# Kernel optimization log

Measured on AMD Instinct MI355X. Metric: run time of the kernel, lower is better.

Reference implementation:

```python
import jax, jax.numpy as jnp
import numpy as np


def _gat(x, edge_index, W, a_src, a_dst, b):
    """PyG-style GATConv (concat=True, negative_slope=0.2, self-loops already in edge_index)."""
    N = x.shape[0]
    H, D = a_src.shape
    src, dst = edge_index[0], edge_index[1]
    h = (x @ W).reshape(N, H, D)                       # [N,H,D]
    alpha_s = jnp.sum(h * a_src, axis=-1)              # [N,H]
    alpha_d = jnp.sum(h * a_dst, axis=-1)              # [N,H]
    e = jax.nn.leaky_relu(alpha_s[src] + alpha_d[dst], 0.2)  # [E,H]
    # segment softmax over incoming edges of each dst node
    m = jax.ops.segment_max(e, dst, num_segments=N)    # [N,H]
    p = jnp.exp(e - m[dst])
    s = jax.ops.segment_sum(p, dst, num_segments=N)
    alpha = p / (s[dst] + 1e-16)                       # [E,H]
    out = jax.ops.segment_sum(h[src] * alpha[:, :, None], dst, num_segments=N)  # [N,H,D]
    return out.reshape(N, H * D) + b


def setup_inputs() -> dict:
    key = jax.random.key(0)
    ks = jax.random.split(key, 16)
    N, E, F_IN, HID, OUT = 50000, 400000, 256, 128, 64

    def glorot(k, shape):
        fan_in, fan_out = shape[0], shape[-1]
        lim = np.sqrt(6.0 / (fan_in + fan_out)).astype(np.float32)
        return jax.random.uniform(k, shape, jnp.float32, -lim, lim)

    return {
        "x": jax.random.normal(ks[0], (N, F_IN), jnp.float32),
        "edge_index": jax.random.randint(ks[1], (2, E), 0, N, jnp.int64),
        "W1": glorot(ks[2], (F_IN, 8 * HID)),
        "as1": glorot(ks[3], (8, HID)),
        "ad1": glorot(ks[4], (8, HID)),
        "b1": jnp.zeros((8 * HID,), jnp.float32),
        "W2": glorot(ks[5], (8 * HID, 4 * HID)),
        "as2": glorot(ks[6], (4, HID)),
        "ad2": glorot(ks[7], (4, HID)),
        "b2": jnp.zeros((4 * HID,), jnp.float32),
        "W3": glorot(ks[8], (4 * HID, OUT)),
        "as3": glorot(ks[9], (1, OUT)),
        "ad3": glorot(ks[10], (1, OUT)),
        "b3": jnp.zeros((OUT,), jnp.float32),
    }


def reference(x, edge_index, W1, as1, ad1, b1, W2, as2, ad2, b2, W3, as3, ad3, b3):
    N = x.shape[0]
    loops = jnp.arange(N, dtype=edge_index.dtype)
    ei = jnp.concatenate([edge_index, jnp.stack([loops, loops])], axis=1)  # add self-loops
    h = jax.nn.elu(_gat(x, ei, W1, as1, ad1, b1))
    h = jax.nn.elu(_gat(h, ei, W2, as2, ad2, b2))
    return _gat(h, ei, W3, as3, ad3, b3)  # task='embedding'
```

## Files before the change

### kernel.cpp

```cpp
#include <hip/hip_runtime.h>
#include <hip/hip_bf16.h>
#include <math.h>


typedef __attribute__((ext_vector_type(8))) short bf16x8;
typedef __attribute__((ext_vector_type(4))) float f32x4;
typedef __attribute__((ext_vector_type(2))) unsigned int u32x2;


__device__ inline float bf2f(unsigned short u) {
    return __uint_as_float(((unsigned int)u) << 16);
}
__device__ inline unsigned short f2bf(float f) {
    unsigned int x = __float_as_uint(f);
    return (unsigned short)((x + 0x7FFFu + ((x >> 16) & 1u)) >> 16);
}
__device__ inline unsigned int pack2bf(float lo, float hi) {
    return (unsigned int)f2bf(lo) | ((unsigned int)f2bf(hi) << 16);
}

template <typename T> __device__ inline float  ldf(const T* p);
template <> __device__ inline float ldf<float>(const float* p) { return *p; }
template <> __device__ inline float ldf<unsigned short>(const unsigned short* p) { return bf2f(*p); }

template <typename T> __device__ inline float4 ld4f(const T* p);
template <> __device__ inline float4 ld4f<float>(const float* p) { return *(const float4*)p; }
template <> __device__ inline float4 ld4f<unsigned short>(const unsigned short* p) {
    short4 v = *(const short4*)p;
    return make_float4(bf2f((unsigned short)v.x), bf2f((unsigned short)v.y),
                       bf2f((unsigned short)v.z), bf2f((unsigned short)v.w));
}

template <typename T> __device__ inline float2 ld2f(const T* p);
template <> __device__ inline float2 ld2f<float>(const float* p) { return *(const float2*)p; }
template <> __device__ inline float2 ld2f<unsigned short>(const unsigned short* p) {
    short2 v = *(const short2*)p;
    return make_float2(bf2f((unsigned short)v.x), bf2f((unsigned short)v.y));
}

template <typename T> __device__ inline void stf(T* p, float v);
template <> __device__ inline void stf<float>(float* p, float v) { *p = v; }
template <> __device__ inline void stf<unsigned short>(unsigned short* p, float v) { *p = f2bf(v); }


__global__ void cvt_bf_kernel(const float* __restrict__ in, unsigned short* __restrict__ out, int n4) {
    int i = blockIdx.x * blockDim.x + threadIdx.x;
    if (i < n4) {
        float4 v = ((const float4*)in)[i];
        short4 s;
        s.x = (short)f2bf(v.x); s.y = (short)f2bf(v.y);
        s.z = (short)f2bf(v.z); s.w = (short)f2bf(v.w);
        ((short4*)out)[i] = s;
    }
}

__global__ void transpose_bf_kernel(const float* __restrict__ W, unsigned short* __restrict__ Wt,
                                    int K, int NOUT) {
    __shared__ float tile[16][17];
    int kb = blockIdx.y * 16, nb = blockIdx.x * 16;
    int tx = threadIdx.x, ty = threadIdx.y;
    tile[ty][tx] = W[(size_t)(kb + ty) * NOUT + nb + tx];
    __syncthreads();
    Wt[(size_t)(nb + ty) * K + kb + tx] = f2bf(tile[tx][ty]);
}


__global__ void count_kernel(const int* __restrict__ ei, int* __restrict__ deg, int E, int N) {
    int i = blockIdx.x * blockDim.x + threadIdx.x;
    if (i < E) {
        int dst = ei[E + i];
        if ((unsigned)dst < (unsigned)N) atomicAdd(&deg[dst], 1);
    }
}

__global__ __launch_bounds__(1024) void scan_kernel(const int* __restrict__ deg,
                                                    int* __restrict__ offs,
                                                    int* __restrict__ cursor, int n) {
    __shared__ int sdata[1024];
    __shared__ int carry_s;
    int tid = threadIdx.x;
    if (tid == 0) carry_s = 0;
    __syncthreads();
    for (int base = 0; base < n; base += 1024) {
        int i = base + tid;
        int v = (i < n) ? (deg[i] + 1) : 0;
        sdata[tid] = v;
        __syncthreads();
        #pragma unroll
        for (int off = 1; off < 1024; off <<= 1) {
            int t = (tid >= off) ? sdata[tid - off] : 0;
            __syncthreads();
            sdata[tid] += t;
            __syncthreads();
        }
        int incl = sdata[tid] + carry_s;
        if (i < n) {
            offs[i + 1] = incl;
            cursor[i] = incl - v;
        }
        __syncthreads();
        if (tid == 1023) carry_s = incl;
        __syncthreads();
    }
    if (tid == 0) offs[0] = 0;
}

__global__ void fill_kernel(const int* __restrict__ ei, int* __restrict__ cursor,
                            int* __restrict__ col, int E, int N) {
    int i = blockIdx.x * blockDim.x + threadIdx.x;
    int cap = E + N;
    if (i < E) {
        int src = ei[i];
        int dst = ei[E + i];
        if ((unsigned)src < (unsigned)N && (unsigned)dst < (unsigned)N) {
            int pos = atomicAdd(&cursor[dst], 1);
            if ((unsigned)pos < (unsigned)cap) col[pos] = src;
        }
    } else if (i < cap) {
        int n = i - E;
        int pos = atomicAdd(&cursor[n], 1);
        if ((unsigned)pos < (unsigned)cap) col[pos] = n;
    }
}


template <int K_, int NOUT, typename TC>
__global__ __launch_bounds__(256) void gemm_mfma(const unsigned short* __restrict__ A,
                                                 const unsigned short* __restrict__ Bt,
                                                 TC* __restrict__ C, int M) {
    constexpr int BM = 128, BN = 128, BK = 64;
    constexpr int LDT = BK + 8;
    __shared__ unsigned short Als[BM][LDT];
    __shared__ unsigned short Bls[BN][LDT];

    int tid = threadIdx.x;
    int lane = tid & 63, wave = tid >> 6;
    int wr = (wave >> 1) * 64, wc = (wave & 1) * 64;
    int row0 = blockIdx.x * BM, col0 = blockIdx.y * BN;

    int sr = tid >> 3;
    int sk = (tid & 7) * 8;

    f32x4 acc[4][4] = {};

    for (int k0 = 0; k0 < K_; k0 += BK) {
        #pragma unroll
        for (int i = 0; i < 4; ++i) {
            int r = sr + i * 32;
            int gr = row0 + r;
            uint4 va = make_uint4(0u, 0u, 0u, 0u);
            if (gr < M) va = *(const uint4*)(A + (size_t)gr * K_ + k0 + sk);
            *(uint4*)&Als[r][sk] = va;
            uint4 vb = *(const uint4*)(Bt + (size_t)(col0 + r) * K_ + k0 + sk);
            *(uint4*)&Bls[r][sk] = vb;
        }
        __syncthreads();
        #pragma unroll
        for (int kh = 0; kh < 2; ++kh) {
            int kk = kh * 32 + (lane >> 4) * 8;
            bf16x8 a[4], b[4];
            #pragma unroll
            for (int m = 0; m < 4; ++m)
                a[m] = *(const bf16x8*)&Als[wr + m * 16 + (lane & 15)][kk];
            #pragma unroll
            for (int n = 0; n < 4; ++n)
                b[n] = *(const bf16x8*)&Bls[wc + n * 16 + (lane & 15)][kk];
            #pragma unroll
            for (int m = 0; m < 4; ++m)
                #pragma unroll
                for (int n = 0; n < 4; ++n)
                    acc[m][n] = __builtin_amdgcn_mfma_f32_16x16x32_bf16(a[m], b[n], acc[m][n], 0, 0, 0);
        }
        __syncthreads();
    }

    int fr = lane & 15, fq = lane >> 4;
    #pragma unroll
    for (int m = 0; m < 4; ++m) {
        #pragma unroll
        for (int j = 0; j < 4; ++j) {
            int r = row0 + wr + m * 16 + fq * 4 + j;
            if (r < M) {
                #pragma unroll
                for (int n = 0; n < 4; ++n)
                    stf(C + (size_t)r * NOUT + col0 + wc + n * 16 + fr, acc[m][n][j]);
            }
        }
    }
}


template <int K_, int NOUT, typename TA, typename TC>
__global__ __launch_bounds__(256) void gemm_kernel(const TA* __restrict__ A,
                                                   const float* __restrict__ B,
                                                   TC* __restrict__ C, int M) {
    constexpr int BM = 128, BN = 64, BK = 16;
    __shared__ float As[BK][BM + 4];
    __shared__ float Bs[BK][BN];

    int tid = threadIdx.x;
    int tx = tid % 16;
    int ty = tid / 16;
    int row0 = blockIdx.x * BM;
    int col0 = blockIdx.y * BN;

    int ar0 = tid / 4;
    int ak  = (tid % 4) * 4;
    int bk  = tid / 16;
    int bn  = (tid % 16) * 4;

    float acc[8][4];
    #pragma unroll
    for (int i = 0; i < 8; ++i)
        #pragma unroll
        for (int j = 0; j < 4; ++j) acc[i][j] = 0.f;

    for (int k0 = 0; k0 < K_; k0 += BK) {
        #pragma unroll
        for (int i = 0; i < 2; ++i) {
            int r = row0 + ar0 + i * 64;
            float4 v = make_float4(0.f, 0.f, 0.f, 0.f);
            if (r < M) v = ld4f(A + (size_t)r * K_ + k0 + ak);
            As[ak + 0][ar0 + i * 64] = v.x;
            As[ak + 1][ar0 + i * 64] = v.y;
            As[ak + 2][ar0 + i * 64] = v.z;
            As[ak + 3][ar0 + i * 64] = v.w;
        }
        float4 w = *(const float4*)(B + (size_t)(k0 + bk) * NOUT + col0 + bn);
        *(float4*)&Bs[bk][bn] = w;
        __syncthreads();

        #pragma unroll
        for (int k = 0; k < BK; ++k) {
            float4 a0 = *(const float4*)&As[k][ty * 8];
            float4 a1 = *(const float4*)&As[k][ty * 8 + 4];
            float4 b0 = *(const float4*)&Bs[k][tx * 4];
            float a[8] = {a0.x, a0.y, a0.z, a0.w, a1.x, a1.y, a1.z, a1.w};
            float b[4] = {b0.x, b0.y, b0.z, b0.w};
            #pragma unroll
            for (int i = 0; i < 8; ++i)
                #pragma unroll
                for (int j = 0; j < 4; ++j) acc[i][j] = fmaf(a[i], b[j], acc[i][j]);
        }
        __syncthreads();
    }

    #pragma unroll
    for (int i = 0; i < 8; ++i) {
        int r = row0 + ty * 8 + i;
        if (r < M) {
            #pragma unroll
            for (int j = 0; j < 4; ++j)
                stf(C + (size_t)r * NOUT + col0 + tx * 4 + j, acc[i][j]);
        }
    }
}


template <int H>
__global__ __launch_bounds__(256) void alpha128_kernel(const unsigned short* __restrict__ h,
                                                       const float* __restrict__ a_src,
                                                       const float* __restrict__ a_dst,
                                                       float* __restrict__ asb,
                                                       float* __restrict__ adb, int N) {
    int node = blockIdx.x * 4 + (threadIdx.x >> 6);
    if (node >= N) return;
    int lane = threadIdx.x & 63;
    const unsigned short* row = h + (size_t)node * (H * 128);
    #pragma unroll
    for (int it = 0; it < H / 4; ++it) {
        int head = it * 4 + (lane >> 4);
        int eoff = it * 512 + (lane >> 4) * 128 + (lane & 15) * 8;
        const unsigned short* p = row + eoff;
        float4 v0 = ld4f(p);
        float4 v1 = ld4f(p + 4);
        const float* asp = a_src + head * 128 + (lane & 15) * 8;
        const float* adp = a_dst + head * 128 + (lane & 15) * 8;
        float4 s0 = *(const float4*)asp, s1 = *(const float4*)(asp + 4);
        float4 d0 = *(const float4*)adp, d1 = *(const float4*)(adp + 4);
        float r1 = v0.x * s0.x + v0.y * s0.y + v0.z * s0.z + v0.w * s0.w
                 + v1.x * s1.x + v1.y * s1.y + v1.z * s1.z + v1.w * s1.w;
        float r2 = v0.x * d0.x + v0.y * d0.y + v0.z * d0.z + v0.w * d0.w
                 + v1.x * d1.x + v1.y * d1.y + v1.z * d1.z + v1.w * d1.w;
        #pragma unroll
        for (int off = 1; off < 16; off <<= 1) {
            r1 += __shfl_xor(r1, off);
            r2 += __shfl_xor(r2, off);
        }
        if ((lane & 15) == 0) {
            asb[node * H + head] = r1;
            adb[node * H + head] = r2;
        }
    }
}

template <int H, int D, typename T>
__global__ __launch_bounds__(256) void alpha_kernel(const T* __restrict__ h,
                                                    const float* __restrict__ a_src,
                                                    const float* __restrict__ a_dst,
                                                    float* __restrict__ as_,
                                                    float* __restrict__ ad_, int N) {
    int wid = blockIdx.x * 4 + threadIdx.x / 64;
    int lane = threadIdx.x % 64;
    if (wid >= N * H) return;
    int n = wid / H, hh = wid % H;
    const T* hrow = h + (size_t)n * (H * D) + hh * D;
    float s1 = 0.f, s2 = 0.f;
    #pragma unroll
    for (int d = lane; d < D; d += 64) {
        float v = ldf(hrow + d);
        s1 = fmaf(v, a_src[hh * D + d], s1);
        s2 = fmaf(v, a_dst[hh * D + d], s2);
    }
    #pragma unroll
    for (int off = 32; off > 0; off >>= 1) {
        s1 += __shfl_down(s1, off);
        s2 += __shfl_down(s2, off);
    }
    if (lane == 0) {
        as_[n * H + hh] = s1;
        ad_[n * H + hh] = s2;
    }
}


template <int H, int D, int BLOCK, bool DO_ELU, typename TIN, typename TOUT>
__global__ __launch_bounds__(BLOCK) void agg_kernel(const TIN* __restrict__ h,
                                                    const float* __restrict__ asb,
                                                    const float* __restrict__ adb,
                                                    const int* __restrict__ offs,
                                                    const int* __restrict__ col,
                                                    const float* __restrict__ bias,
                                                    TOUT* __restrict__ out, int N) {
    constexpr int C = H * D;
    constexpr int V = C / BLOCK;
    constexpr int CH = BLOCK / H;
    __shared__ float e_s[CH][H];
    __shared__ int   col_s[CH];

    int node = blockIdx.x;
    int t = threadIdx.x;
    int c0 = t * V;
    int hh = c0 / D;
    int start = offs[node], end = offs[node + 1];

    int sj = t / H;
    int sh = t % H;
    float adn_stage = adb[node * H + sh];

    float m = -1e30f, ssum = 0.f;
    float acc[V];
    #pragma unroll
    for (int v = 0; v < V; ++v) acc[v] = 0.f;

    for (int base = start; base < end; base += CH) {
        int len = min(CH, end - base);
        __syncthreads();
        if (sj < len) {
            int s = col[base + sj];
            float e;
            if ((unsigned)s < (unsigned)N) {
                e = asb[s * H + sh] + adn_stage;
                e = (e > 0.f) ? e : 0.2f * e;
            } else { e = -1e30f; s = node; }
            e_s[sj][sh] = e;
            if (sh == 0) col_s[sj] = s;
        }
        __syncthreads();

        float cm = -1e30f;
        for (int j = 0; j < len; ++j) cm = fmaxf(cm, e_s[j][hh]);
        float mn = fmaxf(m, cm);
        float scale = __expf(m - mn);
        ssum *= scale;
        #pragma unroll
        for (int v = 0; v < V; ++v) acc[v] *= scale;
        m = mn;

        int j = 0;
        for (; j + 1 < len; j += 2) {
            int s0 = col_s[j], s1 = col_s[j + 1];
            float p0 = __expf(e_s[j][hh] - m);
            float p1 = __expf(e_s[j + 1][hh] - m);
            const TIN* r0 = h + (size_t)s0 * C + c0;
            const TIN* r1 = h + (size_t)s1 * C + c0;
            if constexpr (V == 4) {
                float4 a0 = ld4f(r0), a1 = ld4f(r1);
                acc[0] = fmaf(p0, a0.x, fmaf(p1, a1.x, acc[0]));
                acc[1] = fmaf(p0, a0.y, fmaf(p1, a1.y, acc[1]));
                acc[2] = fmaf(p0, a0.z, fmaf(p1, a1.z, acc[2]));
                acc[3] = fmaf(p0, a0.w, fmaf(p1, a1.w, acc[3]));
            } else if constexpr (V == 2) {
                float2 a0 = ld2f(r0), a1 = ld2f(r1);
                acc[0] = fmaf(p0, a0.x, fmaf(p1, a1.x, acc[0]));
                acc[1] = fmaf(p0, a0.y, fmaf(p1, a1.y, acc[1]));
            } else {
                acc[0] = fmaf(p0, ldf(r0), fmaf(p1, ldf(r1), acc[0]));
            }
            ssum += p0 + p1;
        }
        if (j < len) {
            int s0 = col_s[j];
            float p0 = __expf(e_s[j][hh] - m);
            const TIN* r0 = h + (size_t)s0 * C + c0;
            if constexpr (V == 4) {
                float4 a0 = ld4f(r0);
                acc[0] = fmaf(p0, a0.x, acc[0]);
                acc[1] = fmaf(p0, a0.y, acc[1]);
                acc[2] = fmaf(p0, a0.z, acc[2]);
                acc[3] = fmaf(p0, a0.w, acc[3]);
            } else if constexpr (V == 2) {
                float2 a0 = ld2f(r0);
                acc[0] = fmaf(p0, a0.x, acc[0]);
                acc[1] = fmaf(p0, a0.y, acc[1]);
            } else {
                acc[0] = fmaf(p0, ldf(r0), acc[0]);
            }
            ssum += p0;
        }
    }

    float inv = 1.f / (ssum + 1e-16f);
    float o[V];
    #pragma unroll
    for (int v = 0; v < V; ++v) {
        o[v] = acc[v] * inv + bias[c0 + v];
        if (DO_ELU) o[v] = (o[v] > 0.f) ? o[v] : expm1f(o[v]);
    }
    if constexpr (sizeof(TOUT) == 2) {
        unsigned int* op = (unsigned int*)(out + (size_t)node * C + c0);
        if constexpr (V == 4) {
            u32x2 w;
            w.x = pack2bf(o[0], o[1]);
            w.y = pack2bf(o[2], o[3]);
            __builtin_nontemporal_store(w, (u32x2*)op);
        } else if constexpr (V == 2) {
            __builtin_nontemporal_store(pack2bf(o[0], o[1]), op);
        } else {
            *(unsigned short*)op = f2bf(o[0]);
        }
    } else {
        float* op = (float*)out + (size_t)node * C + c0;
        #pragma unroll
        for (int v = 0; v < V; ++v) __builtin_nontemporal_store(o[v], op + v);
    }
}


extern "C" void kernel_launch(void* const* d_in, const int* in_sizes, int n_in,
                              void* d_out, int out_size, void* d_ws, size_t ws_size,
                              hipStream_t stream) {
    const float* x   = (const float*)d_in[0];
    const int*   ei  = (const int*)d_in[1];
    const float* W1  = (const float*)d_in[2];
    const float* as1 = (const float*)d_in[3];
    const float* ad1 = (const float*)d_in[4];
    const float* b1  = (const float*)d_in[5];
    const float* W2  = (const float*)d_in[6];
    const float* as2 = (const float*)d_in[7];
    const float* ad2 = (const float*)d_in[8];
    const float* b2  = (const float*)d_in[9];
    const float* W3  = (const float*)d_in[10];
    const float* as3 = (const float*)d_in[11];
    const float* ad3 = (const float*)d_in[12];
    const float* b3  = (const float*)d_in[13];
    float*       out = (float*)d_out;

    const int N = in_sizes[0] / 256;
    const int E = in_sizes[1] / 2;

    typedef unsigned short bf;
    size_t off = 0;
    auto alloc = [&](size_t bytes) -> void* {
        void* p = (char*)d_ws + off;
        off += (bytes + 255) & ~(size_t)255;
        return p;
    };
    float* asb    = (float*)alloc((size_t)N * 8 * 4);
    float* adb    = (float*)alloc((size_t)N * 8 * 4);
    int*   deg    = (int*)alloc((size_t)N * 4);
    int*   offs   = (int*)alloc((size_t)(N + 1) * 4);
    int*   cursor = (int*)alloc((size_t)N * 4);
    int*   col    = (int*)alloc((size_t)(E + N) * 4);
    bf*    W1t    = (bf*)alloc((size_t)256 * 1024 * 2);
    bf*    W2t    = (bf*)alloc((size_t)1024 * 512 * 2);
    const size_t NB = (size_t)N * 1024;
    bf* B1 = (bf*)alloc(NB * 2);
    bf* B2 = (bf*)alloc(NB * 2);
    bf* x_bf = B2;

    (void)hipMemsetAsync(deg, 0, (size_t)N * 4, stream);
    count_kernel<<<(E + 255) / 256, 256, 0, stream>>>(ei, deg, E, N);
    scan_kernel<<<1, 1024, 0, stream>>>(deg, offs, cursor, N);
    fill_kernel<<<(E + N + 255) / 256, 256, 0, stream>>>(ei, cursor, col, E, N);

    {
        int n4 = N * 256 / 4;
        cvt_bf_kernel<<<(n4 + 255) / 256, 256, 0, stream>>>(x, x_bf, n4);
        transpose_bf_kernel<<<dim3(1024 / 16, 256 / 16), dim3(16, 16), 0, stream>>>(W1, W1t, 256, 1024);
        transpose_bf_kernel<<<dim3(512 / 16, 1024 / 16), dim3(16, 16), 0, stream>>>(W2, W2t, 1024, 512);
    }

    const int MBm = (N + 127) / 128;
    const int AB  = (N + 3) / 4;

    gemm_mfma<256, 1024, bf><<<dim3(MBm, 8), 256, 0, stream>>>(x_bf, W1t, B1, N);
    alpha128_kernel<8><<<AB, 256, 0, stream>>>(B1, as1, ad1, asb, adb, N);
    agg_kernel<8, 128, 256, true, bf, bf><<<N, 256, 0, stream>>>(B1, asb, adb, offs, col, b1, B2, N);

    gemm_mfma<1024, 512, bf><<<dim3(MBm, 4), 256, 0, stream>>>(B2, W2t, B1, N);
    alpha128_kernel<4><<<AB, 256, 0, stream>>>(B1, as2, ad2, asb, adb, N);
    agg_kernel<4, 128, 256, true, bf, bf><<<N, 256, 0, stream>>>(B1, asb, adb, offs, col, b2, B2, N);

    gemm_kernel<512, 64, bf, bf><<<dim3(MBm, 1), 256, 0, stream>>>(B2, W3, B1, N);
    alpha_kernel<1, 64, bf><<<(N + 3) / 4, 256, 0, stream>>>(B1, as3, ad3, asb, adb, N);
    agg_kernel<1, 64, 64, false, bf, float><<<N, 64, 0, stream>>>(B1, asb, adb, offs, col, b3, out, N);
}
```

Baseline: 848.6 us.

## Precompute segment softmax max and normalizer in separate pass before aggregation

Adds a norm_kernel that computes the per-destination, per-head max and inverse sum of exp in a wavefront-per-node pass. The aggregation kernel then computes normalized attention weights directly during staging, which removes the online-softmax rescaling, the serial max scan over shared memory, and the sum accumulation. The edge loop is also unrolled by four to put more independent gathers in flight. The cost is an extra kernel launch per layer and a second read of col/asb per edge.

Measured after the change: 862.7 us. No clear change (+1.7%).

```diff
diff --git a/kernel.cpp b/kernel.cpp
--- a/kernel.cpp
+++ b/kernel.cpp
@@ -324,10 +324,54 @@
 }
 
 
+template <int H>
+__global__ __launch_bounds__(256) void norm_kernel(const float* __restrict__ asb,
+                                                   const float* __restrict__ adb,
+                                                   const int* __restrict__ offs,
+                                                   const int* __restrict__ col,
+                                                   float* __restrict__ mArr,
+                                                   float* __restrict__ invArr, int N) {
+    int node = blockIdx.x * 4 + (threadIdx.x >> 6);
+    if (node >= N) return;
+    int lane = threadIdx.x & 63;
+    int start = offs[node];
+    int nval = (offs[node + 1] - start) * H;
+    int h = lane % H;
+    float adn = adb[node * H + h];
+
+    float m = -1e30f;
+    for (int i = lane; i < nval; i += 64) {
+        int s = col[start + i / H];
+        float e = asb[s * H + h] + adn;
+        e = (e > 0.f) ? e : 0.2f * e;
+        m = fmaxf(m, e);
+    }
+    #pragma unroll
+    for (int off = H; off < 64; off <<= 1) m = fmaxf(m, __shfl_xor(m, off));
+
+    float ss = 0.f;
+    for (int i = lane; i < nval; i += 64) {
+        int s = col[start + i / H];
+        float e = asb[s * H + h] + adn;
+        e = (e > 0.f) ? e : 0.2f * e;
+        ss += __expf(e - m);
+    }
+    #pragma unroll
+    for (int off = H; off < 64; off <<= 1) ss += __shfl_xor(ss, off);
+
+    if (lane < H) {
+        mArr[node * H + h] = m;
+        invArr[node * H + h] = 1.f / (ss + 1e-16f);
+    }
+}
+
+
 template <int H, int D, int BLOCK, bool DO_ELU, typename TIN, typename TOUT>
 __global__ __launch_bounds__(BLOCK) void agg_kernel(const TIN* __restrict__ h,
                                                     const float* __restrict__ asb,
                                                     const float* __restrict__ adb,
+                                                    const float* __restrict__ mArr,
+                                                    const float* __restrict__ invArr,
                                                     const int* __restrict__ offs,
                                                     const int* __restrict__ col,
                                                     const float* __restrict__ bias,
@@ -335,7 +379,7 @@
     constexpr int C = H * D;
     constexpr int V = C / BLOCK;
     constexpr int CH = BLOCK / H;
-    __shared__ float e_s[CH][H];
+    __shared__ float p_s[CH * H];
     __shared__ int   col_s[CH];
 
     int node = blockIdx.x;
@@ -346,9 +390,10 @@
 
     int sj = t / H;
     int sh = t % H;
-    float adn_stage = adb[node * H + sh];
-
-    float m = -1e30f, ssum = 0.f;
+    float adn_st = adb[node * H + sh];
+    float m_st   = mArr[node * H + sh];
+    float inv_st = invArr[node * H + sh];
+
     float acc[V];
     #pragma unroll
     for (int v = 0; v < V; ++v) acc[v] = 0.f;
@@ -356,52 +401,42 @@
     for (int base = start; base < end; base += CH) {
         int len = min(CH, end - base);
         __syncthreads();
-        if (sj < len) {
+        if (t < len * H) {
             int s = col[base + sj];
-            float e;
-            if ((unsigned)s < (unsigned)N) {
-                e = asb[s * H + sh] + adn_stage;
-                e = (e > 0.f) ? e : 0.2f * e;
-            } else { e = -1e30f; s = node; }
-            e_s[sj][sh] = e;
+            if ((unsigned)s >= (unsigned)N) s = node;
+            float e = asb[s * H + sh] + adn_st;
+            e = (e > 0.f) ? e : 0.2f * e;
+            p_s[t] = __expf(e - m_st) * inv_st;
             if (sh == 0) col_s[sj] = s;
         }
         __syncthreads();
 
-        float cm = -1e30f;
-        for (int j = 0; j < len; ++j) cm = fmaxf(cm, e_s[j][hh]);
-        float mn = fmaxf(m, cm);
-        float scale = __expf(m - mn);
-        ssum *= scale;
-        #pragma unroll
-        for (int v = 0; v < V; ++v) acc[v] *= scale;
-        m = mn;
-
         int j = 0;
-        for (; j + 1 < len; j += 2) {
-            int s0 = col_s[j], s1 = col_s[j + 1];
-            float p0 = __expf(e_s[j][hh] - m);
-            float p1 = __expf(e_s[j + 1][hh] - m);
+        for (; j + 3 < len; j += 4) {
+            int s0 = col_s[j], s1 = col_s[j + 1], s2 = col_s[j + 2], s3 = col_s[j + 3];
+            float p0 = p_s[j * H + hh],       p1 = p_s[(j + 1) * H + hh];
+            float p2 = p_s[(j + 2) * H + hh], p3 = p_s[(j + 3) * H + hh];
             const TIN* r0 = h + (size_t)s0 * C + c0;
             const TIN* r1 = h + (size_t)s1 * C + c0;
+            const TIN* r2 = h + (size_t)s2 * C + c0;
+            const TIN* r3 = h + (size_t)s3 * C + c0;
             if constexpr (V == 4) {
-                float4 a0 = ld4f(r0), a1 = ld4f(r1);
-                acc[0] = fmaf(p0, a0.x, fmaf(p1, a1.x, acc[0]));
-                acc[1] = fmaf(p0, a0.y, fmaf(p1, a1.y, acc[1]));
-                acc[2] = fmaf(p0, a0.z, fmaf(p1, a1.z, acc[2]));
-                acc[3] = fmaf(p0, a0.w, fmaf(p1, a1.w, acc[3]));
+                float4 a0 = ld4f(r0), a1 = ld4f(r1), a2 = ld4f(r2), a3 = ld4f(r3);
+                acc[0] = fmaf(p0, a0.x, fmaf(p1, a1.x, fmaf(p2, a2.x, fmaf(p3, a3.x, acc[0]))));
+                acc[1] = fmaf(p0, a0.y, fmaf(p1, a1.y, fmaf(p2, a2.y, fmaf(p3, a3.y, acc[1]))));
+                acc[2] = fmaf(p0, a0.z, fmaf(p1, a1.z, fmaf(p2, a2.z, fmaf(p3, a3.z, acc[2]))));
+                acc[3] = fmaf(p0, a0.w, fmaf(p1, a1.w, fmaf(p2, a2.w, fmaf(p3, a3.w, acc[3]))));
             } else if constexpr (V == 2) {
-                float2 a0 = ld2f(r0), a1 = ld2f(r1);
-                acc[0] = fmaf(p0, a0.x, fmaf(p1, a1.x, acc[0]));
-                acc[1] = fmaf(p0, a0.y, fmaf(p1, a1.y, acc[1]));
+                float2 a0 = ld2f(r0), a1 = ld2f(r1), a2 = ld2f(r2), a3 = ld2f(r3);
+                acc[0] = fmaf(p0, a0.x, fmaf(p1, a1.x, fmaf(p2, a2.x, fmaf(p3, a3.x, acc[0]))));
+                acc[1] = fmaf(p0, a0.y, fmaf(p1, a1.y, fmaf(p2, a2.y, fmaf(p3, a3.y, acc[1]))));
             } else {
-                acc[0] = fmaf(p0, ldf(r0), fmaf(p1, ldf(r1), acc[0]));
+                acc[0] = fmaf(p0, ldf(r0), fmaf(p1, ldf(r1), fmaf(p2, ldf(r2), fmaf(p3, ldf(r3), acc[0]))));
             }
-            ssum += p0 + p1;
-        }
-        if (j < len) {
+        }
+        for (; j < len; ++j) {
             int s0 = col_s[j];
-            float p0 = __expf(e_s[j][hh] - m);
+            float p0 = p_s[j * H + hh];
             const TIN* r0 = h + (size_t)s0 * C + c0;
             if constexpr (V == 4) {
                 float4 a0 = ld4f(r0);
@@ -416,15 +451,13 @@
             } else {
                 acc[0] = fmaf(p0, ldf(r0), acc[0]);
             }
-            ssum += p0;
-        }
-    }
-
-    float inv = 1.f / (ssum + 1e-16f);
+        }
+    }
+
     float o[V];
     #pragma unroll
     for (int v = 0; v < V; ++v) {
-        o[v] = acc[v] * inv + bias[c0 + v];
+        o[v] = acc[v] + bias[c0 + v];
         if (DO_ELU) o[v] = (o[v] > 0.f) ? o[v] : expm1f(o[v]);
     }
     if constexpr (sizeof(TOUT) == 2) {
@@ -478,6 +511,8 @@
     };
     float* asb    = (float*)alloc((size_t)N * 8 * 4);
     float* adb    = (float*)alloc((size_t)N * 8 * 4);
+    float* mArr   = (float*)alloc((size_t)N * 8 * 4);
+    float* invArr = (float*)alloc((size_t)N * 8 * 4);
     int*   deg    = (int*)alloc((size_t)N * 4);
     int*   offs   = (int*)alloc((size_t)(N + 1) * 4);
     int*   cursor = (int*)alloc((size_t)N * 4);
@@ -506,13 +541,16 @@
 
     gemm_mfma<256, 1024, bf><<<dim3(MBm, 8), 256, 0, stream>>>(x_bf, W1t, B1, N);
     alpha128_kernel<8><<<AB, 256, 0, stream>>>(B1, as1, ad1, asb, adb, N);
-    agg_kernel<8, 128, 256, true, bf, bf><<<N, 256, 0, stream>>>(B1, asb, adb, offs, col, b1, B2, N);
+    norm_kernel<8><<<AB, 256, 0, stream>>>(asb, adb, offs, col, mArr, invArr, N);
+    agg_kernel<8, 128, 256, true, bf, bf><<<N, 256, 0, stream>>>(B1, asb, adb, mArr, invArr, offs, col, b1, B2, N);
 
     gemm_mfma<1024, 512, bf><<<dim3(MBm, 4), 256, 0, stream>>>(B2, W2t, B1, N);
     alpha128_kernel<4><<<AB, 256, 0, stream>>>(B1, as2, ad2, asb, adb, N);
-    agg_kernel<4, 128, 256, true, bf, bf><<<N, 256, 0, stream>>>(B1, asb, adb, offs, col, b2, B2, N);
+    norm_kernel<4><<<AB, 256, 0, stream>>>(asb, adb, offs, col, mArr, invArr, N);
+    agg_kernel<4, 128, 256, true, bf, bf><<<N, 256, 0, stream>>>(B1, asb, adb, mArr, invArr, offs, col, b2, B2, N);
 
     gemm_kernel<512, 64, bf, bf><<<dim3(MBm, 1), 256, 0, stream>>>(B2, W3, B1, N);
     alpha_kernel<1, 64, bf><<<(N + 3) / 4, 256, 0, stream>>>(B1, as3, ad3, asb, adb, N);
-    agg_kernel<1, 64, 64, false, bf, float><<<N, 64, 0, stream>>>(B1, asb, adb, offs, col, b3, out, N);
-}
+    norm_kernel<1><<<AB, 256, 0, stream>>>(asb, adb, offs, col, mArr, invArr, N);
+    agg_kernel<1, 64, 64, false, bf, float><<<N, 64, 0, stream>>>(B1, asb, adb, mArr, invArr, offs, col, b3, out, N);
+}
```
